# Performance work log

Hardware: AMD Instinct MI355X
Metric: run time of the kernel (lower is better)

The kernel has to match this reference:

```python
import jax, jax.numpy as jnp
import numpy as np

T, B, F_, C, H = 500, 16, 32, 64, 64


def _gru(x, h0, w_ih, w_hh, b_ih, b_hh):
    # x: [T, N, C], h0: [N, H]; PyTorch gate order: r, z, n
    xw = x @ w_ih.T + b_ih  # [T, N, 3H] precomputed input projections

    def step(h, xw_t):
        hw = h @ w_hh.T + b_hh
        xr, xz, xn = jnp.split(xw_t, 3, axis=-1)
        hr, hz, hn = jnp.split(hw, 3, axis=-1)
        r = jax.nn.sigmoid(xr + hr)
        z = jax.nn.sigmoid(xz + hz)
        n = jnp.tanh(xn + r * hn)
        h_new = (1.0 - z) * n + z * h
        return h_new, h_new

    hT, ys = jax.lax.scan(step, h0, xw)
    return ys, hT


def setup_inputs() -> dict:
    key = jax.random.key(0)
    ks = jax.random.split(key, 16)
    s = 1.0 / np.sqrt(H)
    inp = {
        "input": jax.random.normal(ks[0], (T, B, F_, C), dtype=jnp.float32),
        "state": jnp.zeros((3, B * F_, H), dtype=jnp.float32),
    }
    i = 1
    for name in ("q", "k", "v"):
        inp[f"w_ih_{name}"] = jax.random.uniform(ks[i], (3 * H, C), jnp.float32, -s, s); i += 1
        inp[f"w_hh_{name}"] = jax.random.uniform(ks[i], (3 * H, H), jnp.float32, -s, s); i += 1
        inp[f"b_ih_{name}"] = jax.random.uniform(ks[i], (3 * H,), jnp.float32, -s, s); i += 1
        inp[f"b_hh_{name}"] = jax.random.uniform(ks[i], (3 * H,), jnp.float32, -s, s); i += 1
    inp["w_o"] = jax.random.uniform(ks[13], (C, H), jnp.float32, -s, s)
    inp["b_o"] = jax.random.uniform(ks[14], (C,), jnp.float32, -s, s)
    return inp


def reference(input, state, w_ih_q, w_hh_q, b_ih_q, b_hh_q,
              w_ih_k, w_hh_k, b_ih_k, b_hh_k,
              w_ih_v, w_hh_v, b_ih_v, b_hh_v, w_o, b_o):
    t, b, f, c = input.shape
    x = input.reshape(t, b * f, c)
    q, h_q = _gru(x, state[0], w_ih_q, w_hh_q, b_ih_q, b_hh_q)
    k, h_k = _gru(x, state[1], w_ih_k, w_hh_k, b_ih_k, b_hh_k)
    v, h_v = _gru(x, state[2], w_ih_v, w_hh_v, b_ih_v, b_hh_v)
    q = q.reshape(t, b, f, H)
    k = k.reshape(t, b, f, H)
    v = v.reshape(t, b, f, H)
    w = jnp.einsum('tbfh,tbgh->tbfg', q, k)        # q @ k^T over freq
    v = jnp.einsum('tbfg,tbgh->tbfh', w, v)        # weights @ v
    v = jax.nn.softmax(v, axis=-2)                 # softmax over freq dim
    o = v @ w_o.T + b_o                            # [t, b, f, c]
    new_state = jnp.stack([h_q, h_k, h_v], axis=0)
    return o, new_state
```

## Files before the change

### kernel.cpp

```cpp
#include <hip/hip_runtime.h>

typedef _Float16 f16x8  __attribute__((ext_vector_type(8)));
typedef float    f32x16 __attribute__((ext_vector_type(16)));

#define TSTEPS 500
#define NB 512
#define LOG2E 1.442695041f

__device__ __forceinline__ double exp_d(double v){
  v = fmin(fmax(v, -700.0), 700.0);
  double t = v * 1.4426950408889634;
  double n = rint(t);
  double f = fma(-n, 6.931471803691238e-01, v);
  f = fma(-n, 1.9082149292705877e-10, f);
  double p = 2.5052108385441718e-08;
  p = fma(p, f, 2.7557319223985893e-07);
  p = fma(p, f, 2.7557319223985888e-06);
  p = fma(p, f, 2.4801587301587302e-05);
  p = fma(p, f, 1.9841269841269841e-04);
  p = fma(p, f, 1.3888888888888889e-03);
  p = fma(p, f, 8.3333333333333332e-03);
  p = fma(p, f, 4.1666666666666664e-02);
  p = fma(p, f, 1.6666666666666666e-01);
  p = fma(p, f, 0.5);
  p = fma(p, f, 1.0);
  p = fma(p, f, 1.0);
  long long bits = (1023LL + (long long)n) << 52;
  return p * __longlong_as_double(bits);
}

__device__ __forceinline__ double rcp_nr(double x){
  double r;
  asm("v_rcp_f64 %0, %1" : "=v"(r) : "v"(x));
  r = fma(fma(-x, r, 1.0), r, r);
  r = fma(fma(-x, r, 1.0), r, r);
  return r;
}

__global__ __launch_bounds__(256, 2) void gru_f64(
    const float* __restrict__ x,
    const float* __restrict__ st,
    const float* __restrict__ wih0, const float* __restrict__ whh0,
    const float* __restrict__ bih0, const float* __restrict__ bhh0,
    const float* __restrict__ wih1, const float* __restrict__ whh1,
    const float* __restrict__ bih1, const float* __restrict__ bhh1,
    const float* __restrict__ wih2, const float* __restrict__ whh2,
    const float* __restrict__ bih2, const float* __restrict__ bhh2,
    _Float16* __restrict__ qkv,
    float* __restrict__ out_state)
{
  __shared__ __align__(16) double hsh[72];
  __shared__ __align__(16) double xsh[72];
  __shared__ __align__(16) double psh[4][72];

  const int tid = threadIdx.x;
  const int j = tid >> 2;
  const int q = tid & 3;
  const int g = blockIdx.x >> 9;
  const int n = blockIdx.x & 511;

  const float* wih = (g==0) ? wih0 : ((g==1) ? wih1 : wih2);
  const float* whh = (g==0) ? whh0 : ((g==1) ? whh1 : whh2);
  const float* bih = (g==0) ? bih0 : ((g==1) ? bih1 : bih2);
  const float* bhh = (g==0) ? bhh0 : ((g==1) ? bhh1 : bhh2);

  double wiR[16], wiZ[16], wiN[16], whR[16], whZ[16], whN[16];
  {
    const float4* pR = (const float4*)(wih + (size_t)(       j)*64 + q*16);
    const float4* pZ = (const float4*)(wih + (size_t)( 64 + j)*64 + q*16);
    const float4* pN = (const float4*)(wih + (size_t)(128 + j)*64 + q*16);
    const float4* rR = (const float4*)(whh + (size_t)(       j)*64 + q*16);
    const float4* rZ = (const float4*)(whh + (size_t)( 64 + j)*64 + q*16);
    const float4* rN = (const float4*)(whh + (size_t)(128 + j)*64 + q*16);
    #pragma unroll
    for (int k=0;k<4;++k){
      float4 a;
      a = pR[k]; wiR[4*k]=(double)a.x; wiR[4*k+1]=(double)a.y; wiR[4*k+2]=(double)a.z; wiR[4*k+3]=(double)a.w;
      a = pZ[k]; wiZ[4*k]=(double)a.x; wiZ[4*k+1]=(double)a.y; wiZ[4*k+2]=(double)a.z; wiZ[4*k+3]=(double)a.w;
      a = pN[k]; wiN[4*k]=(double)a.x; wiN[4*k+1]=(double)a.y; wiN[4*k+2]=(double)a.z; wiN[4*k+3]=(double)a.w;
      a = rR[k]; whR[4*k]=(double)a.x; whR[4*k+1]=(double)a.y; whR[4*k+2]=(double)a.z; whR[4*k+3]=(double)a.w;
      a = rZ[k]; whZ[4*k]=(double)a.x; whZ[4*k+1]=(double)a.y; whZ[4*k+2]=(double)a.z; whZ[4*k+3]=(double)a.w;
      a = rN[k]; whN[4*k]=(double)a.x; whN[4*k+1]=(double)a.y; whN[4*k+2]=(double)a.z; whN[4*k+3]=(double)a.w;
    }
  }
  const double bRi  = (q==0) ? ((double)bih[j]    + (double)bhh[j]   ) : 0.0;
  const double bZi  = (q==0) ? ((double)bih[64+j] + (double)bhh[64+j]) : 0.0;
  const double biNi = (q==0) ? (double)bih[128+j] : 0.0;
  const double bhNi = (q==0) ? (double)bhh[128+j] : 0.0;

  const int l2 = tid & 63;
  const float* xp = x + (size_t)n*64 + l2;

  double h = 0.0;
  float xc0 = 0.f, xc1 = 0.f;
  if (tid < 64){
    h = (double)st[(size_t)(g*512 + n)*64 + tid];
    hsh[tid + 2*(tid>>4)] = h;
  } else if (tid < 128){
    xsh[l2 + 2*(l2>>4)] = (double)xp[0];
    xc0 = xp[(size_t)NB*64];
    xc1 = xp[(size_t)2*NB*64];
  }
  _Float16* qout = qkv + ((size_t)g*TSTEPS*NB + n)*64 + tid;
  __syncthreads();

  for (int t=0; t<TSTEPS; ++t){
    const double2* hp = (const double2*)(&hsh[18*q]);
    const double2* xq = (const double2*)(&xsh[18*q]);

    double hdR=bRi, hdZ=bZi, hdN=bhNi, xdR=0.0, xdZ=0.0, xdN=biNi;
    #pragma unroll
    for (int w=0; w<4; ++w){
      double2 h01 = hp[2*w], h23 = hp[2*w+1];
      double2 x01 = xq[2*w], x23 = xq[2*w+1];
      hdR = fma(whR[4*w+0], h01.x, hdR); hdR = fma(whR[4*w+1], h01.y, hdR);
      hdR = fma(whR[4*w+2], h23.x, hdR); hdR = fma(whR[4*w+3], h23.y, hdR);
      hdZ = fma(whZ[4*w+0], h01.x, hdZ); hdZ = fma(whZ[4*w+1], h01.y, hdZ);
      hdZ = fma(whZ[4*w+2], h23.x, hdZ); hdZ = fma(whZ[4*w+3], h23.y, hdZ);
      hdN = fma(whN[4*w+0], h01.x, hdN); hdN = fma(whN[4*w+1], h01.y, hdN);
      hdN = fma(whN[4*w+2], h23.x, hdN); hdN = fma(whN[4*w+3], h23.y, hdN);
      xdR = fma(wiR[4*w+0], x01.x, xdR); xdR = fma(wiR[4*w+1], x01.y, xdR);
      xdR = fma(wiR[4*w+2], x23.x, xdR); xdR = fma(wiR[4*w+3], x23.y, xdR);
      xdZ = fma(wiZ[4*w+0], x01.x, xdZ); xdZ = fma(wiZ[4*w+1], x01.y, xdZ);
      xdZ = fma(wiZ[4*w+2], x23.x, xdZ); xdZ = fma(wiZ[4*w+3], x23.y, xdZ);
      xdN = fma(wiN[4*w+0], x01.x, xdN); xdN = fma(wiN[4*w+1], x01.y, xdN);
      xdN = fma(wiN[4*w+2], x23.x, xdN); xdN = fma(wiN[4*w+3], x23.y, xdN);
    }
    hdR += __shfl_xor(hdR, 1, 64); hdR += __shfl_xor(hdR, 2, 64);
    hdZ += __shfl_xor(hdZ, 1, 64); hdZ += __shfl_xor(hdZ, 2, 64);
    hdN += __shfl_xor(hdN, 1, 64); hdN += __shfl_xor(hdN, 2, 64);
    xdR += __shfl_xor(xdR, 1, 64); xdR += __shfl_xor(xdR, 2, 64);
    xdZ += __shfl_xor(xdZ, 1, 64); xdZ += __shfl_xor(xdZ, 2, 64);
    xdN += __shfl_xor(xdN, 1, 64); xdN += __shfl_xor(xdN, 2, 64);

    if (q == 0){
      psh[0][j] = hdR + xdR;
      psh[1][j] = hdZ + xdZ;
      psh[2][j] = xdN;
      psh[3][j] = hdN;
    }
    __syncthreads();

    if (tid < 64){
      double aR = psh[0][tid];
      double aZ = psh[1][tid];
      double xn = psh[2][tid];
      double hn = psh[3][tid];
      double r  = rcp_nr(1.0 + exp_d(-aR));
      double z  = rcp_nr(1.0 + exp_d(-aZ));
      double yn = xn + r*hn;
      double nn = 1.0 - 2.0*rcp_nr(exp_d(2.0*yn) + 1.0);
      h = (1.0 - z)*nn + z*h;
      hsh[tid + 2*(tid>>4)] = h;
      qout[(size_t)t*NB*64] = (_Float16)(float)h;
    } else if (tid < 128){
      xsh[l2 + 2*(l2>>4)] = (double)xc0;
      int tp = (t+3 < TSTEPS) ? (t+3) : (TSTEPS-1);
      float xnx = xp[(size_t)tp*NB*64];
      xc0 = xc1; xc1 = xnx;
    }
    __syncthreads();
  }

  if (tid < 64)
    out_state[(size_t)(g*512 + n)*64 + tid] = (float)h;
}

__global__ __launch_bounds__(64) void attn(
    const _Float16* __restrict__ qkv,
    const float* __restrict__ w_o,
    const float* __restrict__ b_o,
    float* __restrict__ out)
{
  __shared__ __align__(16) _Float16 Qs[32*72];
  __shared__ __align__(16) _Float16 Ks[32*72];
  __shared__ __align__(16) _Float16 Vt[64*40];
  __shared__ __align__(16) _Float16 Wm[32*40];
  __shared__ __align__(16) _Float16 wols[64*72];
  __shared__ float bo[64];

  const int lane = threadIdx.x;
  const int t = blockIdx.x >> 4;
  const int b = blockIdx.x & 15;
  const size_t base    = ((size_t)t*NB + b*32)*64;
  const size_t gstride = (size_t)TSTEPS*NB*64;

  #pragma unroll
  for (int it=0; it<4; ++it){
    int idx = it*64 + lane;
    int f = idx >> 3, ko = (idx & 7)*8;
    *(f16x8*)&Qs[f*72+ko] = *(const f16x8*)&qkv[base + (size_t)f*64 + ko];
    *(f16x8*)&Ks[f*72+ko] = *(const f16x8*)&qkv[gstride + base + (size_t)f*64 + ko];
  }
  #pragma unroll
  for (int it=0; it<32; ++it){
    int idx = it*64 + lane;
    int f = idx >> 6, hh = idx & 63;
    Vt[hh*40 + f] = qkv[2*gstride + base + (size_t)f*64 + hh];
  }
  #pragma unroll
  for (int it=0; it<32; ++it){
    int idx = it*64 + lane;
    int c = idx >> 5, hp = (idx & 31)*2;
    float2 u = *(const float2*)(w_o + c*64 + hp);
    wols[c*72 + hp]     = (_Float16)u.x;
    wols[c*72 + hp + 1] = (_Float16)u.y;
  }
  bo[lane] = b_o[lane];

  const int m  = lane & 31;
  const int hk = (lane >> 5) * 8;
  const int rbase = (lane >> 5) * 4;

  f32x16 accW;
  #pragma unroll
  for (int i=0;i<16;++i) accW[i]=0.f;
  #pragma unroll
  for (int kb=0; kb<4; ++kb){
    f16x8 a  = *(const f16x8*)&Qs[m*72 + kb*16 + hk];
    f16x8 bb = *(const f16x8*)&Ks[m*72 + kb*16 + hk];
    accW = __builtin_amdgcn_mfma_f32_32x32x16_f16(a, bb, accW, 0, 0, 0);
  }
  #pragma unroll
  for (int r=0; r<16; ++r){
    int row = (r&3) + 8*(r>>2) + rbase;
    Wm[row*40 + m] = (_Float16)accW[r];
  }

  f32x16 accA0, accA1;
  #pragma unroll
  for (int i=0;i<16;++i){ accA0[i]=0.f; accA1[i]=0.f; }
  #pragma unroll
  for (int kb=0; kb<2; ++kb){
    f16x8 a  = *(const f16x8*)&Wm[m*40 + kb*16 + hk];
    f16x8 b0 = *(const f16x8*)&Vt[(     m)*40 + kb*16 + hk];
    f16x8 b1 = *(const f16x8*)&Vt[(32 + m)*40 + kb*16 + hk];
    accA0 = __builtin_amdgcn_mfma_f32_32x32x16_f16(a, b0, accA0, 0, 0, 0);
    accA1 = __builtin_amdgcn_mfma_f32_32x32x16_f16(a, b1, accA1, 0, 0, 0);
  }

  float mx0 = accA0[0], mx1 = accA1[0];
  #pragma unroll
  for (int r=1;r<16;++r){ mx0 = fmaxf(mx0, accA0[r]); mx1 = fmaxf(mx1, accA1[r]); }
  mx0 = fmaxf(mx0, __shfl_xor(mx0, 32, 64));
  mx1 = fmaxf(mx1, __shfl_xor(mx1, 32, 64));
  float s0 = 0.f, s1 = 0.f;
  #pragma unroll
  for (int r=0;r<16;++r){
    float e0 = __builtin_amdgcn_exp2f(LOG2E*(accA0[r]-mx0)); accA0[r]=e0; s0+=e0;
    float e1 = __builtin_amdgcn_exp2f(LOG2E*(accA1[r]-mx1)); accA1[r]=e1; s1+=e1;
  }
  s0 += __shfl_xor(s0, 32, 64);
  s1 += __shfl_xor(s1, 32, 64);
  float i0 = __builtin_amdgcn_rcpf(s0), i1 = __builtin_amdgcn_rcpf(s1);
  #pragma unroll
  for (int r=0;r<16;++r){
    int row = (r&3) + 8*(r>>2) + rbase;
    Qs[row*72 + m]      = (_Float16)(accA0[r]*i0);
    Qs[row*72 + 32 + m] = (_Float16)(accA1[r]*i1);
  }

  f32x16 accO0, accO1;
  #pragma unroll
  for (int i=0;i<16;++i){ accO0[i]=0.f; accO1[i]=0.f; }
  #pragma unroll
  for (int kb=0; kb<4; ++kb){
    f16x8 a  = *(const f16x8*)&Qs[m*72 + kb*16 + hk];
    f16x8 b0 = *(const f16x8*)&wols[(     m)*72 + kb*16 + hk];
    f16x8 b1 = *(const f16x8*)&wols[(32 + m)*72 + kb*16 + hk];
    accO0 = __builtin_amdgcn_mfma_f32_32x32x16_f16(a, b0, accO0, 0, 0, 0);
    accO1 = __builtin_amdgcn_mfma_f32_32x32x16_f16(a, b1, accO1, 0, 0, 0);
  }
  const size_t obase = ((size_t)t*16 + b)*2048;
  #pragma unroll
  for (int r=0;r<16;++r){
    int row = (r&3) + 8*(r>>2) + rbase;
    out[obase + row*64 + m]      = accO0[r] + bo[m];
    out[obase + row*64 + 32 + m] = accO1[r] + bo[32+m];
  }
}

extern "C" void kernel_launch(void* const* d_in, const int* in_sizes, int n_in,
                              void* d_out, int out_size, void* d_ws, size_t ws_size,
                              hipStream_t stream)
{
  const float* x  = (const float*)d_in[0];
  const float* st = (const float*)d_in[1];
  _Float16* qkv = (_Float16*)d_ws;
  float* out = (float*)d_out;
  float* out_state = out + (size_t)16384000;

  gru_f64<<<dim3(1536), dim3(256), 0, stream>>>(
    x, st,
    (const float*)d_in[2],  (const float*)d_in[3],
    (const float*)d_in[4],  (const float*)d_in[5],
    (const float*)d_in[6],  (const float*)d_in[7],
    (const float*)d_in[8],  (const float*)d_in[9],
    (const float*)d_in[10], (const float*)d_in[11],
    (const float*)d_in[12], (const float*)d_in[13],
    qkv, out_state);

  attn<<<dim3(8000), dim3(64), 0, stream>>>(
    qkv, (const float*)d_in[14], (const float*)d_in[15], out);
}
```

Baseline: 2.177 ms.

## Estrin-form exp polynomial, batch x prefetch by 4 steps, defer h stores

Rewrites the double-precision exp polynomial from Horner form into an Estrin-style evaluation, which shortens the serial dependency chain in the latency-bound recurrence. Unrolls the time loop by 4 and issues the x loads for the next four steps at once, rather than one load per step three steps ahead, so more memory latency can be hidden. The fp16 store of h is moved to the start of the next step, off the critical path after the gate math. This adds registers and changes rounding in exp slightly.

```diff
diff --git a/kernel.cpp b/kernel.cpp
--- a/kernel.cpp
+++ b/kernel.cpp
@@ -10,22 +10,24 @@
 __device__ __forceinline__ double exp_d(double v){
   v = fmin(fmax(v, -700.0), 700.0);
   double t = v * 1.4426950408889634;
-  double n = rint(t);
-  double f = fma(-n, 6.931471803691238e-01, v);
-  f = fma(-n, 1.9082149292705877e-10, f);
-  double p = 2.5052108385441718e-08;
-  p = fma(p, f, 2.7557319223985893e-07);
-  p = fma(p, f, 2.7557319223985888e-06);
-  p = fma(p, f, 2.4801587301587302e-05);
-  p = fma(p, f, 1.9841269841269841e-04);
-  p = fma(p, f, 1.3888888888888889e-03);
-  p = fma(p, f, 8.3333333333333332e-03);
-  p = fma(p, f, 4.1666666666666664e-02);
-  p = fma(p, f, 1.6666666666666666e-01);
-  p = fma(p, f, 0.5);
-  p = fma(p, f, 1.0);
-  p = fma(p, f, 1.0);
-  long long bits = (1023LL + (long long)n) << 52;
+  double nn = rint(t);
+  double f = fma(-nn, 6.931471803691238e-01, v);
+  f = fma(-nn, 1.9082149292705877e-10, f);
+  double f2 = f*f;
+  double f4 = f2*f2;
+  double f8 = f4*f4;
+  double a0 = 1.0 + f;
+  double a1 = fma(f, 1.6666666666666666e-01, 0.5);
+  double a2 = fma(f, 8.3333333333333332e-03, 4.1666666666666664e-02);
+  double a3 = fma(f, 1.9841269841269841e-04, 1.3888888888888889e-03);
+  double a4 = fma(f, 2.7557319223985893e-06, 2.4801587301587302e-05);
+  double a5 = fma(f, 2.5052108385441718e-08, 2.7557319223985888e-07);
+  double b0 = fma(f2, a1, a0);
+  double b1 = fma(f2, a3, a2);
+  double b2 = fma(f2, a5, a4);
+  double p  = fma(f4, b1, b0);
+  p = fma(f8, b2, p);
+  long long bits = (1023LL + (long long)nn) << 52;
   return p * __longlong_as_double(bits);
 }
 
@@ -92,78 +94,100 @@
   const float* xp = x + (size_t)n*64 + l2;
 
   double h = 0.0;
-  float xc0 = 0.f, xc1 = 0.f;
+  float xr0=0.f, xr1=0.f, xr2=0.f, xr3=0.f;
+  float xn0=0.f, xn1=0.f, xn2=0.f, xn3=0.f;
   if (tid < 64){
     h = (double)st[(size_t)(g*512 + n)*64 + tid];
     hsh[tid + 2*(tid>>4)] = h;
   } else if (tid < 128){
     xsh[l2 + 2*(l2>>4)] = (double)xp[0];
-    xc0 = xp[(size_t)NB*64];
-    xc1 = xp[(size_t)2*NB*64];
+    xr0 = xp[(size_t)1*NB*64];
+    xr1 = xp[(size_t)2*NB*64];
+    xr2 = xp[(size_t)3*NB*64];
+    xr3 = xp[(size_t)4*NB*64];
   }
   _Float16* qout = qkv + ((size_t)g*TSTEPS*NB + n)*64 + tid;
   __syncthreads();
 
-  for (int t=0; t<TSTEPS; ++t){
-    const double2* hp = (const double2*)(&hsh[18*q]);
-    const double2* xq = (const double2*)(&xsh[18*q]);
-
-    double hdR=bRi, hdZ=bZi, hdN=bhNi, xdR=0.0, xdZ=0.0, xdN=biNi;
+  for (int t0 = 0; t0 < TSTEPS; t0 += 4){
     #pragma unroll
-    for (int w=0; w<4; ++w){
-      double2 h01 = hp[2*w], h23 = hp[2*w+1];
-      double2 x01 = xq[2*w], x23 = xq[2*w+1];
-      hdR = fma(whR[4*w+0], h01.x, hdR); hdR = fma(whR[4*w+1], h01.y, hdR);
-      hdR = fma(whR[4*w+2], h23.x, hdR); hdR = fma(whR[4*w+3], h23.y, hdR);
-      hdZ = fma(whZ[4*w+0], h01.x, hdZ); hdZ = fma(whZ[4*w+1], h01.y, hdZ);
-      hdZ = fma(whZ[4*w+2], h23.x, hdZ); hdZ = fma(whZ[4*w+3], h23.y, hdZ);
-      hdN = fma(whN[4*w+0], h01.x, hdN); hdN = fma(whN[4*w+1], h01.y, hdN);
-      hdN = fma(whN[4*w+2], h23.x, hdN); hdN = fma(whN[4*w+3], h23.y, hdN);
-      xdR = fma(wiR[4*w+0], x01.x, xdR); xdR = fma(wiR[4*w+1], x01.y, xdR);
-      xdR = fma(wiR[4*w+2], x23.x, xdR); xdR = fma(wiR[4*w+3], x23.y, xdR);
-      xdZ = fma(wiZ[4*w+0], x01.x, xdZ); xdZ = fma(wiZ[4*w+1], x01.y, xdZ);
-      xdZ = fma(wiZ[4*w+2], x23.x, xdZ); xdZ = fma(wiZ[4*w+3], x23.y, xdZ);
-      xdN = fma(wiN[4*w+0], x01.x, xdN); xdN = fma(wiN[4*w+1], x01.y, xdN);
-      xdN = fma(wiN[4*w+2], x23.x, xdN); xdN = fma(wiN[4*w+3], x23.y, xdN);
+    for (int u = 0; u < 4; ++u){
+      const int t = t0 + u;
+
+      if (tid < 64 && t > 0)
+        qout[(size_t)(t-1)*NB*64] = (_Float16)(float)h;
+
+      if (u == 0 && tid >= 64 && tid < 128){
+        int t5 = (t0+5 < TSTEPS) ? (t0+5) : (TSTEPS-1);
+        int t6 = (t0+6 < TSTEPS) ? (t0+6) : (TSTEPS-1);
+        int t7 = (t0+7 < TSTEPS) ? (t0+7) : (TSTEPS-1);
+        int t8 = (t0+8 < TSTEPS) ? (t0+8) : (TSTEPS-1);
+        xn0 = xp[(size_t)t5*NB*64];
+        xn1 = xp[(size_t)t6*NB*64];
+        xn2 = xp[(size_t)t7*NB*64];
+        xn3 = xp[(size_t)t8*NB*64];
+      }
+
+      const double2* hp = (const double2*)(&hsh[18*q]);
+      const double2* xq = (const double2*)(&xsh[18*q]);
+
+      double hdR=bRi, hdZ=bZi, hdN=bhNi, xdR=0.0, xdZ=0.0, xdN=biNi;
+      #pragma unroll
+      for (int w=0; w<4; ++w){
+        double2 h01 = hp[2*w], h23 = hp[2*w+1];
+        double2 x01 = xq[2*w], x23 = xq[2*w+1];
+        hdR = fma(whR[4*w+0], h01.x, hdR); hdR = fma(whR[4*w+1], h01.y, hdR);
+        hdR = fma(whR[4*w+2], h23.x, hdR); hdR = fma(whR[4*w+3], h23.y, hdR);
+        hdZ = fma(whZ[4*w+0], h01.x, hdZ); hdZ = fma(whZ[4*w+1], h01.y, hdZ);
+        hdZ = fma(whZ[4*w+2], h23.x, hdZ); hdZ = fma(whZ[4*w+3], h23.y, hdZ);
+        hdN = fma(whN[4*w+0], h01.x, hdN); hdN = fma(whN[4*w+1], h01.y, hdN);
+        hdN = fma(whN[4*w+2], h23.x, hdN); hdN = fma(whN[4*w+3], h23.y, hdN);
+        xdR = fma(wiR[4*w+0], x01.x, xdR); xdR = fma(wiR[4*w+1], x01.y, xdR);
+        xdR = fma(wiR[4*w+2], x23.x, xdR); xdR = fma(wiR[4*w+3], x23.y, xdR);
+        xdZ = fma(wiZ[4*w+0], x01.x, xdZ); xdZ = fma(wiZ[4*w+1], x01.y, xdZ);
+        xdZ = fma(wiZ[4*w+2], x23.x, xdZ); xdZ = fma(wiZ[4*w+3], x23.y, xdZ);
+        xdN = fma(wiN[4*w+0], x01.x, xdN); xdN = fma(wiN[4*w+1], x01.y, xdN);
+        xdN = fma(wiN[4*w+2], x23.x, xdN); xdN = fma(wiN[4*w+3], x23.y, xdN);
+      }
+      hdR += __shfl_xor(hdR, 1, 64); hdR += __shfl_xor(hdR, 2, 64);
+      hdZ += __shfl_xor(hdZ, 1, 64); hdZ += __shfl_xor(hdZ, 2, 64);
+      hdN += __shfl_xor(hdN, 1, 64); hdN += __shfl_xor(hdN, 2, 64);
+      xdR += __shfl_xor(xdR, 1, 64); xdR += __shfl_xor(xdR, 2, 64);
+      xdZ += __shfl_xor(xdZ, 1, 64); xdZ += __shfl_xor(xdZ, 2, 64);
+      xdN += __shfl_xor(xdN, 1, 64); xdN += __shfl_xor(xdN, 2, 64);
+
+      if (q == 0){
+        psh[0][j] = hdR + xdR;
+        psh[1][j] = hdZ + xdZ;
+        psh[2][j] = xdN;
+        psh[3][j] = hdN;
+      }
+      __syncthreads();
+
+      if (tid < 64){
+        double aR = psh[0][tid];
+        double aZ = psh[1][tid];
+        double xnv = psh[2][tid];
+        double hnv = psh[3][tid];
+        double r  = rcp_nr(1.0 + exp_d(-aR));
+        double z  = rcp_nr(1.0 + exp_d(-aZ));
+        double yn = xnv + r*hnv;
+        double nnv = 1.0 - 2.0*rcp_nr(exp_d(2.0*yn) + 1.0);
+        h = (1.0 - z)*nnv + z*h;
+        hsh[tid + 2*(tid>>4)] = h;
+      } else if (tid < 128){
+        float xs = (u==0) ? xr0 : (u==1) ? xr1 : (u==2) ? xr2 : xr3;
+        xsh[l2 + 2*(l2>>4)] = (double)xs;
+      }
+      __syncthreads();
     }
-    hdR += __shfl_xor(hdR, 1, 64); hdR += __shfl_xor(hdR, 2, 64);
-    hdZ += __shfl_xor(hdZ, 1, 64); hdZ += __shfl_xor(hdZ, 2, 64);
-    hdN += __shfl_xor(hdN, 1, 64); hdN += __shfl_xor(hdN, 2, 64);
-    xdR += __shfl_xor(xdR, 1, 64); xdR += __shfl_xor(xdR, 2, 64);
-    xdZ += __shfl_xor(xdZ, 1, 64); xdZ += __shfl_xor(xdZ, 2, 64);
-    xdN += __shfl_xor(xdN, 1, 64); xdN += __shfl_xor(xdN, 2, 64);
-
-    if (q == 0){
-      psh[0][j] = hdR + xdR;
-      psh[1][j] = hdZ + xdZ;
-      psh[2][j] = xdN;
-      psh[3][j] = hdN;
-    }
-    __syncthreads();
-
-    if (tid < 64){
-      double aR = psh[0][tid];
-      double aZ = psh[1][tid];
-      double xn = psh[2][tid];
-      double hn = psh[3][tid];
-      double r  = rcp_nr(1.0 + exp_d(-aR));
-      double z  = rcp_nr(1.0 + exp_d(-aZ));
-      double yn = xn + r*hn;
-      double nn = 1.0 - 2.0*rcp_nr(exp_d(2.0*yn) + 1.0);
-      h = (1.0 - z)*nn + z*h;
-      hsh[tid + 2*(tid>>4)] = h;
-      qout[(size_t)t*NB*64] = (_Float16)(float)h;
-    } else if (tid < 128){
-      xsh[l2 + 2*(l2>>4)] = (double)xc0;
-      int tp = (t+3 < TSTEPS) ? (t+3) : (TSTEPS-1);
-      float xnx = xp[(size_t)tp*NB*64];
-      xc0 = xc1; xc1 = xnx;
-    }
-    __syncthreads();
-  }
-
-  if (tid < 64)
+    xr0 = xn0; xr1 = xn1; xr2 = xn2; xr3 = xn3;
+  }
+
+  if (tid < 64){
+    qout[(size_t)(TSTEPS-1)*NB*64] = (_Float16)(float)h;
     out_state[(size_t)(g*512 + n)*64 + tid] = (float)h;
+  }
 }
 
 __global__ __launch_bounds__(64) void attn(
```

New measurement: 2.386 ms. 9.6% more time.
